# Kernel tuning notes

Hardware: AMD Instinct MI355X
Metric: run time of the kernel (lower is better)

The kernel has to match this reference:

```python
import jax, jax.numpy as jnp
import numpy as np

EPS = 1e-7

def _dubbed_squash(v):
    norm = jnp.linalg.norm(v, axis=-1, keepdims=True)
    coef = 1.0 - 1.0 / (jnp.exp(norm) + EPS)
    return coef * v / (norm + EPS)

def setup_inputs() -> dict:
    key = jax.random.key(0)
    k1, k2, k3 = jax.random.split(key, 3)
    B, N, dp = 16, 1152, 8   # batch, num_primary_caps, dim_primary_caps
    D, dd = 10, 16           # num_digit_caps, dim_digit_caps
    primary_caps = jax.random.normal(k1, (B, N, dp), dtype=jnp.float32)
    W = jax.random.normal(k2, (D, N, dd, dp), dtype=jnp.float32) * 0.05
    B_prior = jax.random.normal(k3, (D, 1, N), dtype=jnp.float32) * 0.05
    return {"primary_caps": primary_caps, "W": W, "B_prior": B_prior}

def reference(primary_caps, W, B_prior):
    dp = primary_caps.shape[-1]
    # votes: U_hat[b,d,n,j] = W[d,n,j,i] @ u[b,n,i]   (replaces the tf.map_fn)
    U_hat = jnp.einsum('dnji,bni->bdnj', W, primary_caps)  # [B,D,N,dd]
    # self-similarity score matrix (as in original: full NxN matmul)
    A = jnp.einsum('bdnj,bdmj->bdnm', U_hat, U_hat) / jnp.sqrt(
        jnp.asarray(dp, dtype=primary_caps.dtype))          # [B,D,N,N]
    A_sum = jnp.sum(A, axis=2, keepdims=True)               # [B,D,1,N]
    C = jax.nn.softmax(A_sum, axis=1)                       # softmax over digit axis
    # weighted combine with learned log-priors: (B+C) @ U_hat -> [B,D,1,dd] -> squeeze
    S = jnp.einsum('bdkn,bdnj->bdj', B_prior[None] + C, U_hat)  # [B,D,dd]
    return _dubbed_squash(S)
```

## Files before the change

kernel.cpp:

```cpp
#include <hip/hip_runtime.h>

constexpr int BN = 16, NN = 1152, DP = 8, ND = 10, DD = 16;
constexpr int NCH = 2;
constexpr int NBLK = NN / NCH;
constexpr int CELLS = BN * ND * DD;
constexpr int RL = 16;
constexpr int RK = NBLK / RL;
constexpr int WCH = NCH * ND;
constexpr int RBLK = CELLS / RL;
constexpr unsigned MAG1 = 0x7E57C0D1u, MAG2 = 0x7E57C0D2u, MAG3 = 0x7E57C0D3u;
constexpr int SPIN_CAP = 1 << 20;

__device__ __forceinline__ float ld_dev(const float* p) {
    return __hip_atomic_load(p, __ATOMIC_RELAXED, __HIP_MEMORY_SCOPE_AGENT);
}
__device__ __forceinline__ void st_dev(float* p, float v) {
    __hip_atomic_store(p, v, __ATOMIC_RELAXED, __HIP_MEMORY_SCOPE_AGENT);
}

__device__ __forceinline__ void flag_release(unsigned* f, unsigned magic)
{
    __syncthreads();
    if (threadIdx.x == 0)
        __hip_atomic_store(&f[blockIdx.x], magic, __ATOMIC_RELAXED,
                           __HIP_MEMORY_SCOPE_AGENT);
}

__device__ __forceinline__ void flag_wait(const unsigned* f, int nf,
                                          unsigned magic)
{
    for (int i = threadIdx.x; i < nf; i += 256) {
        int spins = 0;
        while (__hip_atomic_load(&f[i], __ATOMIC_RELAXED,
                                 __HIP_MEMORY_SCOPE_AGENT) != magic) {
            __builtin_amdgcn_s_sleep(8);
            if (++spins > SPIN_CAP) break;
        }
    }
    asm volatile("" ::: "memory");
    __syncthreads();
}

__global__ __launch_bounds__(256, 3) void caps_fused(
    const float* __restrict__ u, const float* __restrict__ W,
    const float* __restrict__ Bp, float* __restrict__ Tp,
    float* __restrict__ T, float* __restrict__ Sp,
    unsigned* __restrict__ fl1, unsigned* __restrict__ fl2,
    unsigned* __restrict__ fl3, float* __restrict__ out)
{
    __shared__ float Wl[WCH * 128];
    __shared__ float ul[BN * NCH * DP];
    __shared__ float red[256];

    const int t = threadIdx.x;
    const int blk = blockIdx.x;
    const int n0 = blk * NCH;
    constexpr float RS8 = 0.35355339059327373f;

    for (int g = t; g < WCH * 32; g += 256) {
        const int c = g >> 5, w = g & 31;
        const int nn = c / ND, d = c - nn * ND;
        reinterpret_cast<float4*>(Wl)[g] =
            *reinterpret_cast<const float4*>(
                W + ((size_t)d * NN + (n0 + nn)) * (DD * DP) + w * 4);
    }
    if (t < BN * NCH * 2) {
        const int b = t >> 2, r = t & 3, nn = r >> 1, half = r & 1;
        reinterpret_cast<float4*>(ul)[t] =
            *reinterpret_cast<const float4*>(
                u + ((size_t)b * NN + (n0 + nn)) * DP + half * 4);
    }
    __syncthreads();

    const int j = t & 15, b = t >> 4;

    float uh[NCH][ND];
    float Tacc[ND];
#pragma unroll
    for (int d = 0; d < ND; ++d) Tacc[d] = 0.f;
#pragma unroll
    for (int nn = 0; nn < NCH; ++nn) {
        const float4 u0 = reinterpret_cast<const float4*>(ul)[b * 4 + nn * 2];
        const float4 u1 = reinterpret_cast<const float4*>(ul)[b * 4 + nn * 2 + 1];
#pragma unroll
        for (int d = 0; d < ND; ++d) {
            const float4* wp =
                reinterpret_cast<const float4*>(Wl) + (nn * ND + d) * 32 + j * 2;
            const float4 w0 = wp[0], w1 = wp[1];
            const float s =
                  w0.x * u0.x + w0.y * u0.y + w0.z * u0.z + w0.w * u0.w
                + w1.x * u1.x + w1.y * u1.y + w1.z * u1.z + w1.w * u1.w;
            uh[nn][d] = s;
            Tacc[d] += s;
        }
    }
    {
        float* dst = Tp + (size_t)blk * CELLS;
#pragma unroll
        for (int d = 0; d < ND; ++d) st_dev(dst + d * 256 + t, Tacc[d]);
    }

    flag_release(fl1, MAG1);

    if (blk < RBLK) {
        flag_wait(fl1, NBLK, MAG1);
        const int cell = blk * RL + (t & 15);
        const int cc = t >> 4;
        float v[RK];
#pragma unroll
        for (int k = 0; k < RK; ++k)
            v[k] = ld_dev(Tp + (size_t)(cc + RL * k) * CELLS + cell);
        float s = 0.f;
#pragma unroll
        for (int k = 0; k < RK; ++k) s += v[k];
        red[t] = s;
        __syncthreads();
        if (t < RL) {
            float acc = 0.f;
#pragma unroll
            for (int g = 0; g < RL; ++g) acc += red[t + RL * g];
            st_dev(T + blk * RL + t, acc);
        }
        flag_release(fl2, MAG2);
        flag_wait(fl2, RBLK, MAG2);
    } else {
        flag_wait(fl2, RBLK, MAG2);
    }

    float Treg[ND];
#pragma unroll
    for (int q = 0; q < ND; ++q) Treg[q] = ld_dev(T + q * 256 + t);

    float Sacc[ND];
#pragma unroll
    for (int q = 0; q < ND; ++q) Sacc[q] = 0.f;

#pragma unroll
    for (int nn = 0; nn < NCH; ++nn) {
        const int n = n0 + nn;
        float a[ND];
#pragma unroll
        for (int q = 0; q < ND; ++q) {
            float v = Treg[q] * uh[nn][q];
            v += __shfl_xor(v, 8, 16);
            v += __shfl_xor(v, 4, 16);
            v += __shfl_xor(v, 2, 16);
            v += __shfl_xor(v, 1, 16);
            a[q] = v * RS8;
        }
        float m = a[0];
#pragma unroll
        for (int q = 1; q < ND; ++q) m = fmaxf(m, a[q]);
        float e[ND], se = 0.f;
#pragma unroll
        for (int q = 0; q < ND; ++q) { e[q] = expf(a[q] - m); se += e[q]; }
        const float inv_se = 1.f / se;
#pragma unroll
        for (int q = 0; q < ND; ++q)
            Sacc[q] += (Bp[q * NN + n] + e[q] * inv_se) * uh[nn][q];
    }
    {
        float* dst = Sp + (size_t)blk * CELLS;
#pragma unroll
        for (int q = 0; q < ND; ++q) st_dev(dst + q * 256 + t, Sacc[q]);
    }

    flag_release(fl3, MAG3);

    if (blk < RBLK) {
        flag_wait(fl3, NBLK, MAG3);
        const int q = blk >> 4, bb = blk & 15;
        const int jj = t & 15, cc = t >> 4;
        const int cell = q * 256 + bb * 16 + jj;
        float v[RK];
#pragma unroll
        for (int k = 0; k < RK; ++k)
            v[k] = ld_dev(Sp + (size_t)(cc + RL * k) * CELLS + cell);
        float s = 0.f;
#pragma unroll
        for (int k = 0; k < RK; ++k) s += v[k];
        red[t] = s;
        __syncthreads();
        if (t < RL) {
            float Sv = 0.f;
#pragma unroll
            for (int g = 0; g < RL; ++g) Sv += red[t + RL * g];
            float n2 = Sv * Sv;
#pragma unroll
            for (int off = 8; off >= 1; off >>= 1) n2 += __shfl_xor(n2, off, 16);
            const float nrm = sqrtf(n2);
            const float coef = 1.f - 1.f / (expf(nrm) + 1e-7f);
            out[((size_t)bb * ND + q) * DD + t] = Sv * (coef / (nrm + 1e-7f));
        }
    }
}

extern "C" void kernel_launch(void* const* d_in, const int* in_sizes, int n_in,
                              void* d_out, int out_size, void* d_ws, size_t ws_size,
                              hipStream_t stream) {
    const float* u  = nullptr;
    const float* W  = nullptr;
    const float* Bp = nullptr;
    for (int i = 0; i < n_in; ++i) {
        const int s = in_sizes[i];
        if (s == BN * NN * DP)            u  = (const float*)d_in[i];
        else if (s == ND * NN * DD * DP)  W  = (const float*)d_in[i];
        else if (s == ND * NN)            Bp = (const float*)d_in[i];
    }
    float* out = (float*)d_out;
    char*  wsc = (char*)d_ws;
    float*    Tp  = (float*)wsc;
    float*    T   = Tp + (size_t)NBLK * CELLS;
    float*    Sp  = T + CELLS;
    unsigned* fl1 = (unsigned*)(wsc + (32u << 20));
    unsigned* fl2 = (unsigned*)(wsc + (32u << 20) + 8192);
    unsigned* fl3 = (unsigned*)(wsc + (32u << 20) + 16384);

    caps_fused<<<dim3(NBLK), 256, 0, stream>>>(
        u, W, Bp, Tp, T, Sp, fl1, fl2, fl3, out);
}
```

Baseline: 89.48 us.

## Assign one block per batch-digit pair with local reductions and per-batch sync

Each block now handles one (batch, digit) pair over all primary capsules. It computes votes and the column sum locally, then exchanges only the score row with the 10 blocks of the same batch for the digit softmax. This removes the three grid-wide flag barriers and the partial-sum workspaces. In exchange, the weight slice for each digit is re-read by 16 blocks, only 160 blocks run, and each thread holds many vote registers.

Measured after the change: 113.1 us. +26.5%, slower.

```diff
diff --git a/kernel.cpp b/kernel.cpp
--- a/kernel.cpp
+++ b/kernel.cpp
@@ -1,14 +1,9 @@
 #include <hip/hip_runtime.h>
 
 constexpr int BN = 16, NN = 1152, DP = 8, ND = 10, DD = 16;
-constexpr int NCH = 2;
-constexpr int NBLK = NN / NCH;
-constexpr int CELLS = BN * ND * DD;
-constexpr int RL = 16;
-constexpr int RK = NBLK / RL;
-constexpr int WCH = NCH * ND;
-constexpr int RBLK = CELLS / RL;
-constexpr unsigned MAG1 = 0x7E57C0D1u, MAG2 = 0x7E57C0D2u, MAG3 = 0x7E57C0D3u;
+constexpr int NBLK = BN * ND;
+constexpr int KPT = NN / 16;
+constexpr unsigned MAG1 = 0xC0FFEE01u;
 constexpr int SPIN_CAP = 1 << 20;
 
 __device__ __forceinline__ float ld_dev(const float* p) {
@@ -18,180 +13,118 @@
     __hip_atomic_store(p, v, __ATOMIC_RELAXED, __HIP_MEMORY_SCOPE_AGENT);
 }
 
-__device__ __forceinline__ void flag_release(unsigned* f, unsigned magic)
+__global__ __launch_bounds__(256) void caps_one(
+    const float* __restrict__ u, const float* __restrict__ W,
+    const float* __restrict__ Bp, float* __restrict__ A,
+    unsigned* __restrict__ flags, float* __restrict__ out)
 {
+    __shared__ float ul[NN * DP];
+    __shared__ float coeff[NN];
+    __shared__ float Tpart[16][17];
+    __shared__ float Tl[16];
+    __shared__ float Spart[16][17];
+
+    const int t = threadIdx.x;
+    const int blk = blockIdx.x;
+    const int b = blk / ND, d = blk - b * ND;
+    const int j = t & 15, g = t >> 4;
+    constexpr float RS8 = 0.35355339059327373f;
+
+    {
+        const float4* src = reinterpret_cast<const float4*>(u + (size_t)b * NN * DP);
+        float4* dst4 = reinterpret_cast<float4*>(ul);
+        for (int i = t; i < NN * DP / 4; i += 256) dst4[i] = src[i];
+    }
     __syncthreads();
-    if (threadIdx.x == 0)
-        __hip_atomic_store(&f[blockIdx.x], magic, __ATOMIC_RELAXED,
+
+    float uh[KPT];
+    float tacc = 0.f;
+    const float* Wd = W + (size_t)d * NN * DD * DP;
+#pragma unroll 8
+    for (int k = 0; k < KPT; ++k) {
+        const int n = g + 16 * k;
+        const float4 w0 = *reinterpret_cast<const float4*>(
+            Wd + ((size_t)n * DD + j) * DP);
+        const float4 w1 = *reinterpret_cast<const float4*>(
+            Wd + ((size_t)n * DD + j) * DP + 4);
+        const float4 u0 = reinterpret_cast<const float4*>(ul)[n * 2];
+        const float4 u1 = reinterpret_cast<const float4*>(ul)[n * 2 + 1];
+        const float s = w0.x * u0.x + w0.y * u0.y + w0.z * u0.z + w0.w * u0.w
+                      + w1.x * u1.x + w1.y * u1.y + w1.z * u1.z + w1.w * u1.w;
+        uh[k] = s;
+        tacc += s;
+    }
+
+    Tpart[g][j] = tacc;
+    __syncthreads();
+    if (t < 16) {
+        float s = 0.f;
+#pragma unroll
+        for (int gg = 0; gg < 16; ++gg) s += Tpart[gg][t];
+        Tl[t] = s;
+    }
+    __syncthreads();
+
+    {
+        float* Arow = A + (size_t)blk * NN;
+        const float Tj = Tl[j];
+        for (int k = 0; k < KPT; ++k) {
+            float v = Tj * uh[k];
+            v += __shfl_xor(v, 8, 16);
+            v += __shfl_xor(v, 4, 16);
+            v += __shfl_xor(v, 2, 16);
+            v += __shfl_xor(v, 1, 16);
+            if (j == 0) st_dev(Arow + (g + 16 * k), v * RS8);
+        }
+    }
+
+    __syncthreads();
+    if (t == 0)
+        __hip_atomic_store(&flags[blk], MAG1, __ATOMIC_RELAXED,
                            __HIP_MEMORY_SCOPE_AGENT);
-}
-
-__device__ __forceinline__ void flag_wait(const unsigned* f, int nf,
-                                          unsigned magic)
-{
-    for (int i = threadIdx.x; i < nf; i += 256) {
+    if (t < ND) {
         int spins = 0;
-        while (__hip_atomic_load(&f[i], __ATOMIC_RELAXED,
-                                 __HIP_MEMORY_SCOPE_AGENT) != magic) {
-            __builtin_amdgcn_s_sleep(8);
+        while (__hip_atomic_load(&flags[b * ND + t], __ATOMIC_RELAXED,
+                                 __HIP_MEMORY_SCOPE_AGENT) != MAG1) {
+            __builtin_amdgcn_s_sleep(2);
             if (++spins > SPIN_CAP) break;
         }
     }
     asm volatile("" ::: "memory");
     __syncthreads();
-}
 
-__global__ __launch_bounds__(256, 3) void caps_fused(
-    const float* __restrict__ u, const float* __restrict__ W,
-    const float* __restrict__ Bp, float* __restrict__ Tp,
-    float* __restrict__ T, float* __restrict__ Sp,
-    unsigned* __restrict__ fl1, unsigned* __restrict__ fl2,
-    unsigned* __restrict__ fl3, float* __restrict__ out)
-{
-    __shared__ float Wl[WCH * 128];
-    __shared__ float ul[BN * NCH * DP];
-    __shared__ float red[256];
-
-    const int t = threadIdx.x;
-    const int blk = blockIdx.x;
-    const int n0 = blk * NCH;
-    constexpr float RS8 = 0.35355339059327373f;
-
-    for (int g = t; g < WCH * 32; g += 256) {
-        const int c = g >> 5, w = g & 31;
-        const int nn = c / ND, d = c - nn * ND;
-        reinterpret_cast<float4*>(Wl)[g] =
-            *reinterpret_cast<const float4*>(
-                W + ((size_t)d * NN + (n0 + nn)) * (DD * DP) + w * 4);
-    }
-    if (t < BN * NCH * 2) {
-        const int b = t >> 2, r = t & 3, nn = r >> 1, half = r & 1;
-        reinterpret_cast<float4*>(ul)[t] =
-            *reinterpret_cast<const float4*>(
-                u + ((size_t)b * NN + (n0 + nn)) * DP + half * 4);
+    {
+        const float* Ab = A + (size_t)b * ND * NN;
+        for (int n = t; n < NN; n += 256) {
+            float aq[ND];
+#pragma unroll
+            for (int q = 0; q < ND; ++q) aq[q] = ld_dev(Ab + (size_t)q * NN + n);
+            float m = aq[0];
+#pragma unroll
+            for (int q = 1; q < ND; ++q) m = fmaxf(m, aq[q]);
+            float se = 0.f;
+#pragma unroll
+            for (int q = 0; q < ND; ++q) { aq[q] = expf(aq[q] - m); se += aq[q]; }
+            coeff[n] = Bp[(size_t)d * NN + n] + aq[d] / se;
+        }
     }
     __syncthreads();
 
-    const int j = t & 15, b = t >> 4;
-
-    float uh[NCH][ND];
-    float Tacc[ND];
+    float sacc = 0.f;
+#pragma unroll 8
+    for (int k = 0; k < KPT; ++k) sacc += coeff[g + 16 * k] * uh[k];
+    Spart[g][j] = sacc;
+    __syncthreads();
+    if (t < 16) {
+        float Sv = 0.f;
 #pragma unroll
-    for (int d = 0; d < ND; ++d) Tacc[d] = 0.f;
+        for (int gg = 0; gg < 16; ++gg) Sv += Spart[gg][t];
+        float n2 = Sv * Sv;
 #pragma unroll
-    for (int nn = 0; nn < NCH; ++nn) {
-        const float4 u0 = reinterpret_cast<const float4*>(ul)[b * 4 + nn * 2];
-        const float4 u1 = reinterpret_cast<const float4*>(ul)[b * 4 + nn * 2 + 1];
-#pragma unroll
-        for (int d = 0; d < ND; ++d) {
-            const float4* wp =
-                reinterpret_cast<const float4*>(Wl) + (nn * ND + d) * 32 + j * 2;
-            const float4 w0 = wp[0], w1 = wp[1];
-            const float s =
-                  w0.x * u0.x + w0.y * u0.y + w0.z * u0.z + w0.w * u0.w
-                + w1.x * u1.x + w1.y * u1.y + w1.z * u1.z + w1.w * u1.w;
-            uh[nn][d] = s;
-            Tacc[d] += s;
-        }
-    }
-    {
-        float* dst = Tp + (size_t)blk * CELLS;
-#pragma unroll
-        for (int d = 0; d < ND; ++d) st_dev(dst + d * 256 + t, Tacc[d]);
-    }
-
-    flag_release(fl1, MAG1);
-
-    if (blk < RBLK) {
-        flag_wait(fl1, NBLK, MAG1);
-        const int cell = blk * RL + (t & 15);
-        const int cc = t >> 4;
-        float v[RK];
-#pragma unroll
-        for (int k = 0; k < RK; ++k)
-            v[k] = ld_dev(Tp + (size_t)(cc + RL * k) * CELLS + cell);
-        float s = 0.f;
-#pragma unroll
-        for (int k = 0; k < RK; ++k) s += v[k];
-        red[t] = s;
-        __syncthreads();
-        if (t < RL) {
-            float acc = 0.f;
-#pragma unroll
-            for (int g = 0; g < RL; ++g) acc += red[t + RL * g];
-            st_dev(T + blk * RL + t, acc);
-        }
-        flag_release(fl2, MAG2);
-        flag_wait(fl2, RBLK, MAG2);
-    } else {
-        flag_wait(fl2, RBLK, MAG2);
-    }
-
-    float Treg[ND];
-#pragma unroll
-    for (int q = 0; q < ND; ++q) Treg[q] = ld_dev(T + q * 256 + t);
-
-    float Sacc[ND];
-#pragma unroll
-    for (int q = 0; q < ND; ++q) Sacc[q] = 0.f;
-
-#pragma unroll
-    for (int nn = 0; nn < NCH; ++nn) {
-        const int n = n0 + nn;
-        float a[ND];
-#pragma unroll
-        for (int q = 0; q < ND; ++q) {
-            float v = Treg[q] * uh[nn][q];
-            v += __shfl_xor(v, 8, 16);
-            v += __shfl_xor(v, 4, 16);
-            v += __shfl_xor(v, 2, 16);
-            v += __shfl_xor(v, 1, 16);
-            a[q] = v * RS8;
-        }
-        float m = a[0];
-#pragma unroll
-        for (int q = 1; q < ND; ++q) m = fmaxf(m, a[q]);
-        float e[ND], se = 0.f;
-#pragma unroll
-        for (int q = 0; q < ND; ++q) { e[q] = expf(a[q] - m); se += e[q]; }
-        const float inv_se = 1.f / se;
-#pragma unroll
-        for (int q = 0; q < ND; ++q)
-            Sacc[q] += (Bp[q * NN + n] + e[q] * inv_se) * uh[nn][q];
-    }
-    {
-        float* dst = Sp + (size_t)blk * CELLS;
-#pragma unroll
-        for (int q = 0; q < ND; ++q) st_dev(dst + q * 256 + t, Sacc[q]);
-    }
-
-    flag_release(fl3, MAG3);
-
-    if (blk < RBLK) {
-        flag_wait(fl3, NBLK, MAG3);
-        const int q = blk >> 4, bb = blk & 15;
-        const int jj = t & 15, cc = t >> 4;
-        const int cell = q * 256 + bb * 16 + jj;
-        float v[RK];
-#pragma unroll
-        for (int k = 0; k < RK; ++k)
-            v[k] = ld_dev(Sp + (size_t)(cc + RL * k) * CELLS + cell);
-        float s = 0.f;
-#pragma unroll
-        for (int k = 0; k < RK; ++k) s += v[k];
-        red[t] = s;
-        __syncthreads();
-        if (t < RL) {
-            float Sv = 0.f;
-#pragma unroll
-            for (int g = 0; g < RL; ++g) Sv += red[t + RL * g];
-            float n2 = Sv * Sv;
-#pragma unroll
-            for (int off = 8; off >= 1; off >>= 1) n2 += __shfl_xor(n2, off, 16);
-            const float nrm = sqrtf(n2);
-            const float coef = 1.f - 1.f / (expf(nrm) + 1e-7f);
-            out[((size_t)bb * ND + q) * DD + t] = Sv * (coef / (nrm + 1e-7f));
-        }
+        for (int off = 8; off >= 1; off >>= 1) n2 += __shfl_xor(n2, off, 16);
+        const float nrm = sqrtf(n2);
+        const float coef = 1.f - 1.f / (expf(nrm) + 1e-7f);
+        out[((size_t)b * ND + d) * DD + t] = Sv * (coef / (nrm + 1e-7f));
     }
 }
 
@@ -209,13 +142,8 @@
     }
     float* out = (float*)d_out;
     char*  wsc = (char*)d_ws;
-    float*    Tp  = (float*)wsc;
-    float*    T   = Tp + (size_t)NBLK * CELLS;
-    float*    Sp  = T + CELLS;
-    unsigned* fl1 = (unsigned*)(wsc + (32u << 20));
-    unsigned* fl2 = (unsigned*)(wsc + (32u << 20) + 8192);
-    unsigned* fl3 = (unsigned*)(wsc + (32u << 20) + 16384);
+    float*    A     = (float*)wsc;
+    unsigned* flags = (unsigned*)(wsc + (1u << 20));
 
-    caps_fused<<<dim3(NBLK), 256, 0, stream>>>(
-        u, W, Bp, Tp, T, Sp, fl1, fl2, fl3, out);
+    caps_one<<<dim3(NBLK), 256, 0, stream>>>(u, W, Bp, A, flags, out);
 }
```
